# Performance work log

Measured on AMD Instinct MI355X. Metric: run time of the kernel, lower is better.

The kernel has to match this reference:

```python
import jax, jax.numpy as jnp
import numpy as np

RELU_SCALE = 0.25  # const power-of-two activation scale for QuantReLU (uint4)
DN = ('NCHW', 'OIHW', 'NCHW')
BN_EPS = 1e-5


def ste_round(x):
    # straight-through-estimator round (brevitas RoundSte)
    return x + jax.lax.stop_gradient(jnp.round(x) - x)


def fq_signed(x, bits):
    # per-tensor symmetric fixed-point fake quant with power-of-two scale
    # (Int8WeightPerTensorFixedPoint / Int8ActPerTensorFixedPoint at bit_width=bits)
    n = 2.0 ** (bits - 1) - 1.0
    m = jnp.maximum(jnp.max(jnp.abs(x)), 1e-8)
    s = jax.lax.stop_gradient(jnp.exp2(jnp.ceil(jnp.log2(m / n))))
    return jnp.clip(ste_round(x / s), -n - 1.0, n) * s


def quant_relu4(x):
    # QuantReLU: uint4, CONST power-of-two scale
    return jnp.clip(ste_round(x / RELU_SCALE), 0.0, 15.0) * RELU_SCALE


def bn(x, g, b, m, v):
    # inference-form BatchNorm2d (running stats)
    inv = g * jax.lax.rsqrt(v + BN_EPS)
    return x * inv[None, :, None, None] + (b - m * inv)[None, :, None, None]


def qconv(x, w, stride, groups):
    # QuantConv2d: fake-quant input (int4) and weight (int4), then conv
    xq = fq_signed(x, 4)
    wq = fq_signed(w, 4)
    pad = 'VALID' if w.shape[-1] == 1 else ((1, 1), (1, 1))
    return jax.lax.conv_general_dilated(
        xq, wq, (stride, stride), pad,
        dimension_numbers=DN, feature_group_count=groups)


def setup_inputs() -> dict:
    key = jax.random.key(0)
    ks = jax.random.split(key, 24)
    B, Cin, H, W = 32, 64, 56, 56
    expansion, Cout = 6, 96
    P = expansion * Cin  # 384

    def bn_params(i, C):
        g = jax.random.uniform(ks[i], (C,), minval=0.5, maxval=1.5)
        b = jax.random.normal(ks[i + 1], (C,)) * 0.1
        m = jax.random.normal(ks[i + 2], (C,)) * 0.1
        v = jax.random.uniform(ks[i + 3], (C,), minval=0.5, maxval=1.5)
        return g, b, m, v

    x = jax.random.normal(ks[0], (B, Cin, H, W), dtype=jnp.float32)
    w1 = jax.random.normal(ks[1], (P, Cin, 1, 1), dtype=jnp.float32) * 0.1
    w2 = jax.random.normal(ks[2], (P, 1, 3, 3), dtype=jnp.float32) * 0.1
    w3 = jax.random.normal(ks[3], (Cout, P, 1, 1), dtype=jnp.float32) * 0.1
    ws = jax.random.normal(ks[4], (Cout, Cin, 1, 1), dtype=jnp.float32) * 0.1
    g1, b1, m1, v1 = bn_params(5, P)
    g2, b2, m2, v2 = bn_params(9, P)
    g3, b3, m3, v3 = bn_params(13, Cout)
    gs, bs, ms, vs = bn_params(17, Cout)
    return {
        'x': x,
        'w1': w1, 'g1': g1, 'b1': b1, 'm1': m1, 'v1': v1,
        'w2': w2, 'g2': g2, 'b2': b2, 'm2': m2, 'v2': v2,
        'w3': w3, 'g3': g3, 'b3': b3, 'm3': m3, 'v3': v3,
        'ws': ws, 'gs': gs, 'bs': bs, 'ms': ms, 'vs': vs,
    }


def reference(x, w1, g1, b1, m1, v1, w2, g2, b2, m2, v2,
              w3, g3, b3, m3, v3, ws, gs, bs, ms, vs):
    P = w1.shape[0]
    # expand 1x1 -> BN -> QuantReLU
    out = quant_relu4(bn(qconv(x, w1, 1, 1), g1, b1, m1, v1))
    # depthwise 3x3 (stride=1) -> BN -> QuantReLU
    out = quant_relu4(bn(qconv(out, w2, 1, P), g2, b2, m2, v2))
    # project 1x1 with int8 output_quant -> BN
    out = bn(fq_signed(qconv(out, w3, 1, 1), 8), g3, b3, m3, v3)
    # shortcut: 1x1 quant conv (int4 output_quant) -> BN  (stride==1, Cin!=Cout)
    sc = bn(fq_signed(qconv(x, ws, 1, 1), 4), gs, bs, ms, vs)
    return quant_relu4(out + sc)
```

## Files before the change

### kernel.cpp

```cpp
#include <hip/hip_runtime.h>
#include <stdint.h>

#define B_  32
#define CIN 64
#define H_  56
#define W_  56
#define HW_ 3136
#define P_  384
#define CO_ 96

__device__ __forceinline__ float pot_scale(float m, float n) {
    float q = fmaxf(m, 1e-8f) / n;
    int e; float f = frexpf(q, &e);
    return ldexpf(1.0f, (f == 0.5f) ? (e - 1) : e);
}

__device__ __forceinline__ int dot8(int a, int b, int c) {
#if __has_builtin(__builtin_amdgcn_sdot8)
    return __builtin_amdgcn_sdot8(a, b, c, false);
#else
#pragma unroll
    for (int j = 0; j < 8; j++) {
        int av = (a << (28 - 4 * j)) >> 28;
        int bv = (b << (28 - 4 * j)) >> 28;
        c += av * bv;
    }
    return c;
#endif
}

__device__ __forceinline__ int iclamp(int v, int lo, int hi) { return min(max(v, lo), hi); }

__device__ __forceinline__ unsigned build_lut(float r, int lo) {
    unsigned v = 0;
#pragma unroll
    for (int L = 0; L < 8; L++)
        v |= (unsigned)min((int)rintf(__fmul_rn((float)(lo + L), r)), 7) << (4 * L);
    return v;
}
__device__ __forceinline__ int lut1(unsigned lo, unsigned hi, int L) {
    unsigned sel = (L & 8) ? hi : lo;
    return (int)((sel >> ((L & 7) * 4)) & 7u);
}
__device__ __forceinline__ unsigned lutn4(unsigned lo, unsigned hi, unsigned v) {
    return (unsigned)lut1(lo, hi, (int)(v & 0xffu))
         | ((unsigned)lut1(lo, hi, (int)((v >> 8) & 0xffu)) << 4)
         | ((unsigned)lut1(lo, hi, (int)((v >> 16) & 0xffu)) << 8)
         | ((unsigned)lut1(lo, hi, (int)((v >> 24) & 0xffu)) << 12);
}

__device__ __forceinline__ int block_max(int v, int* red) {
    int tid = threadIdx.x;
    red[tid] = v; __syncthreads();
    for (int s = 128; s > 0; s >>= 1) {
        if (tid < s) red[tid] = max(red[tid], red[tid + s]);
        __syncthreads();
    }
    int r = red[0];
    __syncthreads();
    return r;
}


__global__ __launch_bounds__(1024) void k_init_bn(
    float* sf, float* bnb,
    const float* g1, const float* b1, const float* m1, const float* v1,
    const float* g2, const float* b2, const float* m2, const float* v2,
    const float* g3, const float* b3, const float* m3, const float* v3,
    const float* gs, const float* bs, const float* ms, const float* vs)
{
    int t = threadIdx.x;
    if (t < 32) ((int*)sf)[t] = 0;
    if (t < 384) {
        float inv = __fmul_rn(g1[t], __fdiv_rn(1.0f, sqrtf(__fadd_rn(v1[t], 1e-5f))));
        bnb[t] = inv;
        bnb[384 + t] = __fsub_rn(b1[t], __fmul_rn(m1[t], inv));
    } else if (t < 768) {
        int i = t - 384;
        float inv = __fmul_rn(g2[i], __fdiv_rn(1.0f, sqrtf(__fadd_rn(v2[i], 1e-5f))));
        bnb[768 + i] = inv;
        bnb[1152 + i] = __fsub_rn(b2[i], __fmul_rn(m2[i], inv));
    } else if (t < 864) {
        int i = t - 768;
        float inv = __fmul_rn(g3[i], __fdiv_rn(1.0f, sqrtf(__fadd_rn(v3[i], 1e-5f))));
        bnb[1536 + i] = inv;
        bnb[1632 + i] = __fsub_rn(b3[i], __fmul_rn(m3[i], inv));
    } else if (t < 960) {
        int i = t - 864;
        float inv = __fmul_rn(gs[i], __fdiv_rn(1.0f, sqrtf(__fadd_rn(vs[i], 1e-5f))));
        bnb[1728 + i] = inv;
        bnb[1824 + i] = __fsub_rn(bs[i], __fmul_rn(ms[i], inv));
    }
}

__global__ __launch_bounds__(256) void k_maxes(
    const float* __restrict__ x, const float* __restrict__ w1,
    const float* __restrict__ w2, const float* __restrict__ w3,
    const float* __restrict__ wsc, float* sf)
{
    __shared__ int red[256];
    int tid = threadIdx.x;
    float m = 0.f;
    if (blockIdx.x < 512) {
        const float4* x4 = (const float4*)x;
        const int n4 = (B_ * CIN * HW_) / 4;
        for (int i = blockIdx.x * 256 + tid; i < n4; i += 512 * 256) {
            float4 v = x4[i];
            m = fmaxf(m, fmaxf(fmaxf(fabsf(v.x), fabsf(v.y)),
                               fmaxf(fabsf(v.z), fabsf(v.w))));
        }
        int bm = block_max(__float_as_int(m), red);
        if (tid == 0) atomicMax((int*)&sf[0], bm);
    } else {
        int seg = blockIdx.x - 512;
        const float* p = seg == 0 ? w1 : seg == 1 ? w2 : seg == 2 ? w3 : wsc;
        int n = seg == 0 ? P_ * CIN : seg == 1 ? P_ * 9 : seg == 2 ? CO_ * P_ : CO_ * CIN;
        for (int i = tid; i < n; i += 256) m = fmaxf(m, fabsf(p[i]));
        int bm = block_max(__float_as_int(m), red);
        if (tid == 0) atomicMax((int*)&sf[1 + seg], bm);
    }
}

__global__ __launch_bounds__(256) void k_quantx(
    const float* __restrict__ x, const float* __restrict__ sf, int* __restrict__ xq4)
{
    int flat = blockIdx.x * 256 + threadIdx.x;
    float rx = 1.0f / pot_scale(sf[0], 7.0f);
    int hw = flat % HW_;
    int c8 = (flat / HW_) & 7;
    int b  = flat / (8 * HW_);
    const float* xp = x + (size_t)(b * 64 + c8 * 8) * HW_ + hw;
    unsigned pk = 0;
#pragma unroll
    for (int j = 0; j < 8; j++) {
        int q = iclamp((int)rintf(__fmul_rn(xp[(size_t)j * HW_], rx)), -8, 7);
        pk |= (unsigned)(q & 0xF) << (4 * j);
    }
    xq4[flat] = (int)pk;
}

__global__ __launch_bounds__(256) void k_quantw(
    const float* __restrict__ w1, const float* __restrict__ w2,
    const float* __restrict__ w3, const float* __restrict__ wsc,
    const float* __restrict__ sf,
    int* __restrict__ w1n, int8_t* __restrict__ w2q,
    int* __restrict__ w3n, int* __restrict__ wsn)
{
    int flat = blockIdx.x * 256 + threadIdx.x;
    if (flat < 3072) {
        int d = flat, co = d & 3, k8 = (d >> 2) & 7, g = d >> 5;
        float r = 1.0f / pot_scale(sf[1], 7.f);
        const float* src = w1 + (4 * g + co) * 64 + 8 * k8;
        unsigned pk = 0;
#pragma unroll
        for (int j = 0; j < 8; j++) {
            int q = iclamp((int)rintf(__fmul_rn(src[j], r)), -8, 7);
            pk |= (unsigned)(q & 0xF) << (4 * j);
        }
        w1n[d] = (int)pk;
    } else if (flat < 7680) {
        int d = flat - 3072, co = d & 3, k8 = (d >> 2) % 48, coq = d / 192;
        float r = 1.0f / pot_scale(sf[3], 7.f);
        const float* src = w3 + (4 * coq + co) * 384 + 8 * k8;
        unsigned pk = 0;
#pragma unroll
        for (int j = 0; j < 8; j++) {
            int q = iclamp((int)rintf(__fmul_rn(src[j], r)), -8, 7);
            pk |= (unsigned)(q & 0xF) << (4 * j);
        }
        w3n[d] = (int)pk;
    } else if (flat < 8448) {
        int d = flat - 7680, co = d & 3, k8 = (d >> 2) & 7, coq = d >> 5;
        float r = 1.0f / pot_scale(sf[4], 7.f);
        const float* src = wsc + (4 * coq + co) * 64 + 8 * k8;
        unsigned pk = 0;
#pragma unroll
        for (int j = 0; j < 8; j++) {
            int q = iclamp((int)rintf(__fmul_rn(src[j], r)), -8, 7);
            pk |= (unsigned)(q & 0xF) << (4 * j);
        }
        wsn[d] = (int)pk;
    } else if (flat < 11904) {
        int i = flat - 8448;
        float r = 1.0f / pot_scale(sf[2], 7.f);
        w2q[i] = (int8_t)iclamp((int)rintf(__fmul_rn(w2[i], r)), -8, 7);
    }
}

__global__ __launch_bounds__(256) void k_conv1(
    const int* __restrict__ xq4, const int4* __restrict__ w1n,
    const int4* __restrict__ wsn,
    const float* __restrict__ sf, const float* __restrict__ bnb,
    unsigned* __restrict__ out1p, int* si)
{
    __shared__ __align__(16) int xs[8 * W_];
    __shared__ int red[256];
    int tid = threadIdx.x;
    int b = blockIdx.x / H_, h = blockIdx.x % H_;
    for (int i = tid; i < 8 * W_; i += 256)
        xs[i] = xq4[((b * 8 + i / W_) * HW_) + h * W_ + (i % W_)];
    float sprod = __fmul_rn(pot_scale(sf[0], 7.f), pot_scale(sf[1], 7.f));
    __syncthreads();
    int lmax = 0;
    for (int qi = tid; qi < 96 * 14; qi += 256) {
        int g = qi / 14, w4 = (qi % 14) * 4;
        int acc[4][4];
#pragma unroll
        for (int c = 0; c < 4; c++)
#pragma unroll
            for (int w = 0; w < 4; w++) acc[c][w] = 0;
        const int4* wp = w1n + g * 8;
#pragma unroll
        for (int k = 0; k < 8; k++) {
            int4 wv = wp[k];
            int4 xv = *(const int4*)&xs[k * W_ + w4];
            acc[0][0] = dot8(xv.x, wv.x, acc[0][0]); acc[0][1] = dot8(xv.y, wv.x, acc[0][1]);
            acc[0][2] = dot8(xv.z, wv.x, acc[0][2]); acc[0][3] = dot8(xv.w, wv.x, acc[0][3]);
            acc[1][0] = dot8(xv.x, wv.y, acc[1][0]); acc[1][1] = dot8(xv.y, wv.y, acc[1][1]);
            acc[1][2] = dot8(xv.z, wv.y, acc[1][2]); acc[1][3] = dot8(xv.w, wv.y, acc[1][3]);
            acc[2][0] = dot8(xv.x, wv.z, acc[2][0]); acc[2][1] = dot8(xv.y, wv.z, acc[2][1]);
            acc[2][2] = dot8(xv.z, wv.z, acc[2][2]); acc[2][3] = dot8(xv.w, wv.z, acc[2][3]);
            acc[3][0] = dot8(xv.x, wv.w, acc[3][0]); acc[3][1] = dot8(xv.y, wv.w, acc[3][1]);
            acc[3][2] = dot8(xv.z, wv.w, acc[3][2]); acc[3][3] = dot8(xv.w, wv.w, acc[3][3]);
        }
        float4 invv = *(const float4*)&bnb[4 * g];
        float4 betv = *(const float4*)&bnb[384 + 4 * g];
        float inva[4] = {invv.x, invv.y, invv.z, invv.w};
        float beta[4] = {betv.x, betv.y, betv.z, betv.w};
        uint4 ov;
        unsigned* op = (unsigned*)&ov;
#pragma unroll
        for (int w = 0; w < 4; w++) {
            unsigned pkd = 0;
#pragma unroll
            for (int c = 0; c < 4; c++) {
                float y = __fadd_rn(__fmul_rn(__fmul_rn((float)acc[c][w], sprod), inva[c]), beta[c]);
                int L = iclamp((int)rintf(__fmul_rn(y, 4.f)), 0, 15);
                lmax = max(lmax, L);
                pkd |= (unsigned)L << (8 * c);
            }
            op[w] = pkd;
        }
        *(uint4*)(out1p + (size_t)(b * 96 + g) * HW_ + h * W_ + w4) = ov;
    }
    int bm = block_max(lmax, red);
    if (tid == 0) atomicMax(&si[5], bm);
    int amax = 0;
    for (int qi = tid; qi < 24 * 14; qi += 256) {
        int coq = qi / 14, w4 = (qi % 14) * 4;
        int acc[4][4];
#pragma unroll
        for (int c = 0; c < 4; c++)
#pragma unroll
            for (int w = 0; w < 4; w++) acc[c][w] = 0;
        const int4* wp = wsn + coq * 8;
#pragma unroll
        for (int k = 0; k < 8; k++) {
            int4 wv = wp[k];
            int4 xv = *(const int4*)&xs[k * W_ + w4];
            acc[0][0] = dot8(xv.x, wv.x, acc[0][0]); acc[0][1] = dot8(xv.y, wv.x, acc[0][1]);
            acc[0][2] = dot8(xv.z, wv.x, acc[0][2]); acc[0][3] = dot8(xv.w, wv.x, acc[0][3]);
            acc[1][0] = dot8(xv.x, wv.y, acc[1][0]); acc[1][1] = dot8(xv.y, wv.y, acc[1][1]);
            acc[1][2] = dot8(xv.z, wv.y, acc[1][2]); acc[1][3] = dot8(xv.w, wv.y, acc[1][3]);
            acc[2][0] = dot8(xv.x, wv.z, acc[2][0]); acc[2][1] = dot8(xv.y, wv.z, acc[2][1]);
            acc[2][2] = dot8(xv.z, wv.z, acc[2][2]); acc[2][3] = dot8(xv.w, wv.z, acc[2][3]);
            acc[3][0] = dot8(xv.x, wv.w, acc[3][0]); acc[3][1] = dot8(xv.y, wv.w, acc[3][1]);
            acc[3][2] = dot8(xv.z, wv.w, acc[3][2]); acc[3][3] = dot8(xv.w, wv.w, acc[3][3]);
        }
#pragma unroll
        for (int c = 0; c < 4; c++)
            amax = max(amax, max(max(abs(acc[c][0]), abs(acc[c][1])),
                                 max(abs(acc[c][2]), abs(acc[c][3]))));
    }
    bm = block_max(amax, red);
    if (tid == 0) atomicMax(&si[8], bm);
}

__global__ __launch_bounds__(256) void k_conv2(
    const unsigned* __restrict__ out1p, const int8_t* __restrict__ w2q,
    const float* __restrict__ sf, int* si,
    const float* __restrict__ bnb, unsigned* __restrict__ out2p)
{
    __shared__ int plane[58 * 58];
    __shared__ int red[256];
    int tid = threadIdx.x;
    int b = blockIdx.x / 96, g = blockIdx.x % 96;
    float s_a2 = pot_scale(0.25f * (float)si[5], 7.f);
    float r2 = 0.25f / s_a2;
    float sprod = __fmul_rn(s_a2, pot_scale(sf[2], 7.f));
    unsigned lutlo = build_lut(r2, 0), luthi = build_lut(r2, 8);
    const unsigned* src = out1p + (size_t)(b * 96 + g) * HW_;
    for (int i = tid; i < 58 * 58; i += 256) {
        int r = i / 58, c = i % 58;
        int pv = 0;
        if (r >= 1 && r <= 56 && c >= 1 && c <= 56) {
            unsigned v = src[(r - 1) * W_ + (c - 1)];
            pv = lut1(lutlo, luthi, (int)(v & 0xffu))
               | (lut1(lutlo, luthi, (int)((v >> 8) & 0xffu)) << 8)
               | (lut1(lutlo, luthi, (int)((v >> 16) & 0xffu)) << 16)
               | (lut1(lutlo, luthi, (int)((v >> 24) & 0xffu)) << 24);
        }
        plane[i] = pv;
    }
    int wv[4][9];
#pragma unroll
    for (int c = 0; c < 4; c++)
#pragma unroll
        for (int t = 0; t < 9; t++) wv[c][t] = (int)w2q[(4 * g + c) * 9 + t];
    float4 invv = *(const float4*)&bnb[768 + 4 * g];
    float4 betv = *(const float4*)&bnb[1152 + 4 * g];
    float inva[4] = {invv.x, invv.y, invv.z, invv.w};
    float beta[4] = {betv.x, betv.y, betv.z, betv.w};
    __syncthreads();
    int lmax = 0;
    unsigned* dst = out2p + (size_t)(b * 96 + g) * HW_;
    for (int i = tid; i < HW_; i += 256) {
        int oh = i / W_, ow = i % W_;
        int acc[4] = {0, 0, 0, 0};
#pragma unroll
        for (int j = 0; j < 3; j++) {
#pragma unroll
            for (int l = 0; l < 3; l++) {
                int pv = plane[(oh + j) * 58 + ow + l];
                int t = j * 3 + l;
                acc[0] += (pv & 0xff)         * wv[0][t];
                acc[1] += ((pv >> 8) & 0xff)  * wv[1][t];
                acc[2] += ((pv >> 16) & 0xff) * wv[2][t];
                acc[3] += ((pv >> 24) & 0xff) * wv[3][t];
            }
        }
        unsigned pkd = 0;
#pragma unroll
        for (int c = 0; c < 4; c++) {
            float y = __fadd_rn(__fmul_rn(__fmul_rn((float)acc[c], sprod), inva[c]), beta[c]);
            int L = iclamp((int)rintf(__fmul_rn(y, 4.f)), 0, 15);
            lmax = max(lmax, L);
            pkd |= (unsigned)L << (8 * c);
        }
        dst[i] = pkd;
    }
    int bm = block_max(lmax, red);
    if (tid == 0) atomicMax(&si[6], bm);
}

__global__ __launch_bounds__(256) void k_conv3(
    const unsigned* __restrict__ out2p, const int4* __restrict__ w3n,
    const float* __restrict__ sf, int* si,
    int16_t* __restrict__ acc3)
{
    __shared__ __align__(16) int a3s[2 * 48 * W_];
    __shared__ int red[256];
    int tid = threadIdx.x;
    int b = blockIdx.x / 28, h0 = (blockIdx.x % 28) * 2;
    float s_a3 = pot_scale(0.25f * (float)si[6], 7.f);
    float r3 = 0.25f / s_a3;
    unsigned lutlo = build_lut(r3, 0), luthi = build_lut(r3, 8);
    for (int i = tid; i < 2 * 48 * W_; i += 256) {
        int row = i / (48 * W_), rem = i % (48 * W_), c8 = rem / W_, w = rem % W_;
        size_t base = (size_t)(b * 96 + c8 * 2) * HW_ + (h0 + row) * W_ + w;
        unsigned v0 = out2p[base], v1 = out2p[base + HW_];
        a3s[i] = (int)(lutn4(lutlo, luthi, v0) | (lutn4(lutlo, luthi, v1) << 16));
    }
    __syncthreads();
    int amax = 0;
    for (int qi = tid; qi < 672; qi += 256) {
        int row = qi / 336, rem2 = qi % 336, coq = rem2 / 14, w4 = (rem2 % 14) * 4;
        int acc[4][4];
#pragma unroll
        for (int c = 0; c < 4; c++)
#pragma unroll
            for (int w = 0; w < 4; w++) acc[c][w] = 0;
        const int4* wp = w3n + coq * 48;
        const int* ap = a3s + row * 48 * W_ + w4;
#pragma unroll 6
        for (int k = 0; k < 48; k++) {
            int4 wv = wp[k];
            int4 av = *(const int4*)(ap + k * W_);
            acc[0][0] = dot8(av.x, wv.x, acc[0][0]); acc[0][1] = dot8(av.y, wv.x, acc[0][1]);
            acc[0][2] = dot8(av.z, wv.x, acc[0][2]); acc[0][3] = dot8(av.w, wv.x, acc[0][3]);
            acc[1][0] = dot8(av.x, wv.y, acc[1][0]); acc[1][1] = dot8(av.y, wv.y, acc[1][1]);
            acc[1][2] = dot8(av.z, wv.y, acc[1][2]); acc[1][3] = dot8(av.w, wv.y, acc[1][3]);
            acc[2][0] = dot8(av.x, wv.z, acc[2][0]); acc[2][1] = dot8(av.y, wv.z, acc[2][1]);
            acc[2][2] = dot8(av.z, wv.z, acc[2][2]); acc[2][3] = dot8(av.w, wv.z, acc[2][3]);
            acc[3][0] = dot8(av.x, wv.w, acc[3][0]); acc[3][1] = dot8(av.y, wv.w, acc[3][1]);
            acc[3][2] = dot8(av.z, wv.w, acc[3][2]); acc[3][3] = dot8(av.w, wv.w, acc[3][3]);
        }
#pragma unroll
        for (int c = 0; c < 4; c++) {
            int co = coq * 4 + c;
            amax = max(amax, max(max(abs(acc[c][0]), abs(acc[c][1])),
                                 max(abs(acc[c][2]), abs(acc[c][3]))));
            short4 st = make_short4((short)acc[c][0], (short)acc[c][1],
                                    (short)acc[c][2], (short)acc[c][3]);
            *(short4*)(acc3 + (size_t)(b * CO_ + co) * HW_ + (h0 + row) * W_ + w4) = st;
        }
    }
    int bm = block_max(amax, red);
    if (tid == 0) atomicMax(&si[7], bm);
}

__global__ __launch_bounds__(256) void k_final(
    const int* __restrict__ xq4, const int4* __restrict__ wsn,
    const int16_t* __restrict__ acc3, const float* __restrict__ sf,
    const int* __restrict__ si, const float* __restrict__ bnb,
    float* __restrict__ dout)
{
    __shared__ __align__(16) int xs[8 * W_];
    int tid = threadIdx.x;
    int b = blockIdx.x / H_, h = blockIdx.x % H_;
    for (int i = tid; i < 8 * W_; i += 256)
        xs[i] = xq4[((b * 8 + i / W_) * HW_) + h * W_ + (i % W_)];
    float s_a3   = pot_scale(0.25f * (float)si[6], 7.f);
    float sprod3 = __fmul_rn(s_a3, pot_scale(sf[3], 7.f));
    float s_q3   = pot_scale(__fmul_rn(sprod3, (float)si[7]), 127.f);
    float rq3    = sprod3 / s_q3;
    float sprods = __fmul_rn(pot_scale(sf[0], 7.f), pot_scale(sf[4], 7.f));
    float s_qs   = pot_scale(__fmul_rn(sprods, (float)si[8]), 7.f);
    float rqs    = sprods / s_qs;
    __syncthreads();
    for (int qi = tid; qi < 24 * 14; qi += 256) {
        int coq = qi / 14, w4 = (qi % 14) * 4;
        int acc[4][4];
#pragma unroll
        for (int c = 0; c < 4; c++)
#pragma unroll
            for (int w = 0; w < 4; w++) acc[c][w] = 0;
        const int4* wp = wsn + coq * 8;
#pragma unroll
        for (int k = 0; k < 8; k++) {
            int4 wv = wp[k];
            int4 xv = *(const int4*)&xs[k * W_ + w4];
            acc[0][0] = dot8(xv.x, wv.x, acc[0][0]); acc[0][1] = dot8(xv.y, wv.x, acc[0][1]);
            acc[0][2] = dot8(xv.z, wv.x, acc[0][2]); acc[0][3] = dot8(xv.w, wv.x, acc[0][3]);
            acc[1][0] = dot8(xv.x, wv.y, acc[1][0]); acc[1][1] = dot8(xv.y, wv.y, acc[1][1]);
            acc[1][2] = dot8(xv.z, wv.y, acc[1][2]); acc[1][3] = dot8(xv.w, wv.y, acc[1][3]);
            acc[2][0] = dot8(xv.x, wv.z, acc[2][0]); acc[2][1] = dot8(xv.y, wv.z, acc[2][1]);
            acc[2][2] = dot8(xv.z, wv.z, acc[2][2]); acc[2][3] = dot8(xv.w, wv.z, acc[2][3]);
            acc[3][0] = dot8(xv.x, wv.w, acc[3][0]); acc[3][1] = dot8(xv.y, wv.w, acc[3][1]);
            acc[3][2] = dot8(xv.z, wv.w, acc[3][2]); acc[3][3] = dot8(xv.w, wv.w, acc[3][3]);
        }
        float4 inv3v = *(const float4*)&bnb[1536 + 4 * coq];
        float4 bet3v = *(const float4*)&bnb[1632 + 4 * coq];
        float4 invSv = *(const float4*)&bnb[1728 + 4 * coq];
        float4 betSv = *(const float4*)&bnb[1824 + 4 * coq];
        float inv3a[4] = {inv3v.x, inv3v.y, inv3v.z, inv3v.w};
        float bet3a[4] = {bet3v.x, bet3v.y, bet3v.z, bet3v.w};
        float invSa[4] = {invSv.x, invSv.y, invSv.z, invSv.w};
        float betSa[4] = {betSv.x, betSv.y, betSv.z, betSv.w};
#pragma unroll
        for (int c = 0; c < 4; c++) {
            int co = coq * 4 + c;
            size_t idx = (size_t)(b * CO_ + co) * HW_ + h * W_ + w4;
            short4 c3 = *(const short4*)(acc3 + idx);
            int c3a[4] = {c3.x, c3.y, c3.z, c3.w};
            float4 o4;
            float* o = (float*)&o4;
#pragma unroll
            for (int j = 0; j < 4; j++) {
                int q3 = iclamp((int)rintf(__fmul_rn((float)c3a[j], rq3)), -128, 127);
                float y3 = __fadd_rn(__fmul_rn(__fmul_rn((float)q3, s_q3), inv3a[c]), bet3a[c]);
                int qs = iclamp((int)rintf(__fmul_rn((float)acc[c][j], rqs)), -8, 7);
                float ys = __fadd_rn(__fmul_rn(__fmul_rn((float)qs, s_qs), invSa[c]), betSa[c]);
                float oo = __fadd_rn(y3, ys);
                int L = iclamp((int)rintf(__fmul_rn(oo, 4.f)), 0, 15);
                o[j] = (float)L * 0.25f;
            }
            *(float4*)(dout + idx) = o4;
        }
    }
}

extern "C" void kernel_launch(void* const* d_in, const int* in_sizes, int n_in,
                              void* d_out, int out_size, void* d_ws, size_t ws_size,
                              hipStream_t stream)
{
    const float* x   = (const float*)d_in[0];
    const float* w1  = (const float*)d_in[1];
    const float* g1  = (const float*)d_in[2];
    const float* b1  = (const float*)d_in[3];
    const float* m1  = (const float*)d_in[4];
    const float* v1  = (const float*)d_in[5];
    const float* w2  = (const float*)d_in[6];
    const float* g2  = (const float*)d_in[7];
    const float* b2  = (const float*)d_in[8];
    const float* m2  = (const float*)d_in[9];
    const float* v2  = (const float*)d_in[10];
    const float* w3  = (const float*)d_in[11];
    const float* g3  = (const float*)d_in[12];
    const float* b3  = (const float*)d_in[13];
    const float* m3  = (const float*)d_in[14];
    const float* v3  = (const float*)d_in[15];
    const float* wsc = (const float*)d_in[16];
    const float* gs  = (const float*)d_in[17];
    const float* bs  = (const float*)d_in[18];
    const float* ms  = (const float*)d_in[19];
    const float* vs  = (const float*)d_in[20];

    char* ws = (char*)d_ws;
    float*    sf    = (float*)ws;
    int*      si    = (int*)ws;
    float*    bnb   = (float*)(ws + 256);
    int*      w1n   = (int*)(ws + 8192);
    int8_t*   w2q   = (int8_t*)(ws + 32768);
    int*      w3n   = (int*)(ws + 36864);
    int*      wsn   = (int*)(ws + 73728);
    int*      xq4   = (int*)(ws + (1u << 20));
    unsigned* out1p = (unsigned*)(ws + (8u << 20));
    int16_t*  acc3  = (int16_t*)(ws + (8u << 20));
    unsigned* out2p = (unsigned*)(ws + (48u << 20));

    k_init_bn<<<1, 1024, 0, stream>>>(sf, bnb, g1, b1, m1, v1, g2, b2, m2, v2,
                                      g3, b3, m3, v3, gs, bs, ms, vs);
    k_maxes<<<516, 256, 0, stream>>>(x, w1, w2, w3, wsc, sf);
    k_quantx<<<3136, 256, 0, stream>>>(x, sf, xq4);
    k_quantw<<<47, 256, 0, stream>>>(w1, w2, w3, wsc, sf, w1n, w2q, w3n, wsn);
    k_conv1<<<B_ * H_, 256, 0, stream>>>(xq4, (const int4*)w1n, (const int4*)wsn,
                                         sf, bnb, out1p, si);
    k_conv2<<<B_ * 96, 256, 0, stream>>>(out1p, w2q, sf, si, bnb, out2p);
    k_conv3<<<B_ * 28, 256, 0, stream>>>(out2p, (const int4*)w3n, sf, si, acc3);
    k_final<<<B_ * H_, 256, 0, stream>>>(xq4, (const int4*)wsn, acc3, sf, si, bnb,
                                         (float*)d_out);
}
```

Measured before the change: 305.1 us.

## Retile conv1/conv2 work, vectorize x quantization, widen max-reduction grid

Several kernels are reworked at once. k_maxes launches more blocks over x. k_quantx handles four pixels per thread with float4 loads and int4 stores. k_conv1 now runs 192 threads, each keeping its group's weights and BN params in registers across seven pixel quads, with a reduction variant that zero-pads the unused shared slots. k_conv2 gives each thread a column and slides a 3x3 register window down rows to reuse loads, and k_conv3 reorders its work index so neighbouring threads share weights. The aim is fewer redundant global and shared loads, at the cost of idle lanes (ow>=56) and extra register use.

```diff
diff --git a/kernel.cpp b/kernel.cpp
--- a/kernel.cpp
+++ b/kernel.cpp
@@ -52,6 +52,20 @@
 __device__ __forceinline__ int block_max(int v, int* red) {
     int tid = threadIdx.x;
     red[tid] = v; __syncthreads();
+    for (int s = 128; s > 0; s >>= 1) {
+        if (tid < s) red[tid] = max(red[tid], red[tid + s]);
+        __syncthreads();
+    }
+    int r = red[0];
+    __syncthreads();
+    return r;
+}
+
+__device__ __forceinline__ int block_max192(int v, int* red) {
+    int tid = threadIdx.x;
+    red[tid] = v;
+    if (tid < 64) red[192 + tid] = 0;
+    __syncthreads();
     for (int s = 128; s > 0; s >>= 1) {
         if (tid < s) red[tid] = max(red[tid], red[tid + s]);
         __syncthreads();
@@ -93,6 +107,7 @@
     }
 }
 
+#define XBLK 2044
 __global__ __launch_bounds__(256) void k_maxes(
     const float* __restrict__ x, const float* __restrict__ w1,
     const float* __restrict__ w2, const float* __restrict__ w3,
@@ -101,10 +116,10 @@
     __shared__ int red[256];
     int tid = threadIdx.x;
     float m = 0.f;
-    if (blockIdx.x < 512) {
+    if (blockIdx.x < XBLK) {
         const float4* x4 = (const float4*)x;
         const int n4 = (B_ * CIN * HW_) / 4;
-        for (int i = blockIdx.x * 256 + tid; i < n4; i += 512 * 256) {
+        for (int i = blockIdx.x * 256 + tid; i < n4; i += XBLK * 256) {
             float4 v = x4[i];
             m = fmaxf(m, fmaxf(fmaxf(fabsf(v.x), fabsf(v.y)),
                                fmaxf(fabsf(v.z), fabsf(v.w))));
@@ -112,7 +127,7 @@
         int bm = block_max(__float_as_int(m), red);
         if (tid == 0) atomicMax((int*)&sf[0], bm);
     } else {
-        int seg = blockIdx.x - 512;
+        int seg = blockIdx.x - XBLK;
         const float* p = seg == 0 ? w1 : seg == 1 ? w2 : seg == 2 ? w3 : wsc;
         int n = seg == 0 ? P_ * CIN : seg == 1 ? P_ * 9 : seg == 2 ? CO_ * P_ : CO_ * CIN;
         for (int i = tid; i < n; i += 256) m = fmaxf(m, fabsf(p[i]));
@@ -124,19 +139,25 @@
 __global__ __launch_bounds__(256) void k_quantx(
     const float* __restrict__ x, const float* __restrict__ sf, int* __restrict__ xq4)
 {
-    int flat = blockIdx.x * 256 + threadIdx.x;
+    int t = blockIdx.x * 256 + threadIdx.x;
     float rx = 1.0f / pot_scale(sf[0], 7.0f);
-    int hw = flat % HW_;
-    int c8 = (flat / HW_) & 7;
-    int b  = flat / (8 * HW_);
-    const float* xp = x + (size_t)(b * 64 + c8 * 8) * HW_ + hw;
-    unsigned pk = 0;
+    int hw4 = (t % 784) * 4;
+    int c8  = (t / 784) & 7;
+    int b   = t / (784 * 8);
+    const float* xp = x + (size_t)(b * 64 + c8 * 8) * HW_ + hw4;
+    unsigned pk[4] = {0, 0, 0, 0};
 #pragma unroll
     for (int j = 0; j < 8; j++) {
-        int q = iclamp((int)rintf(__fmul_rn(xp[(size_t)j * HW_], rx)), -8, 7);
-        pk |= (unsigned)(q & 0xF) << (4 * j);
-    }
-    xq4[flat] = (int)pk;
+        float4 v = *(const float4*)(xp + (size_t)j * HW_);
+        float va[4] = {v.x, v.y, v.z, v.w};
+#pragma unroll
+        for (int w = 0; w < 4; w++) {
+            int q = iclamp((int)rintf(__fmul_rn(va[w], rx)), -8, 7);
+            pk[w] |= (unsigned)(q & 0xF) << (4 * j);
+        }
+    }
+    int4 st = make_int4((int)pk[0], (int)pk[1], (int)pk[2], (int)pk[3]);
+    *(int4*)(xq4 + (size_t)(b * 8 + c8) * HW_ + hw4) = st;
 }
 
 __global__ __launch_bounds__(256) void k_quantw(
@@ -187,7 +208,7 @@
     }
 }
 
-__global__ __launch_bounds__(256) void k_conv1(
+__global__ __launch_bounds__(192) void k_conv1(
     const int* __restrict__ xq4, const int4* __restrict__ w1n,
     const int4* __restrict__ wsn,
     const float* __restrict__ sf, const float* __restrict__ bnb,
@@ -197,19 +218,71 @@
     __shared__ int red[256];
     int tid = threadIdx.x;
     int b = blockIdx.x / H_, h = blockIdx.x % H_;
-    for (int i = tid; i < 8 * W_; i += 256)
+    for (int i = tid; i < 8 * W_; i += 192)
         xs[i] = xq4[((b * 8 + i / W_) * HW_) + h * W_ + (i % W_)];
     float sprod = __fmul_rn(pot_scale(sf[0], 7.f), pot_scale(sf[1], 7.f));
     __syncthreads();
+    int g = tid % 96, half = tid / 96;
+    int4 wreg[8];
+    {
+        const int4* wp = w1n + g * 8;
+#pragma unroll
+        for (int k = 0; k < 8; k++) wreg[k] = wp[k];
+    }
+    float4 invv = *(const float4*)&bnb[4 * g];
+    float4 betv = *(const float4*)&bnb[384 + 4 * g];
+    float inva[4] = {invv.x, invv.y, invv.z, invv.w};
+    float beta[4] = {betv.x, betv.y, betv.z, betv.w};
     int lmax = 0;
-    for (int qi = tid; qi < 96 * 14; qi += 256) {
-        int g = qi / 14, w4 = (qi % 14) * 4;
+    unsigned* dst = out1p + (size_t)(b * 96 + g) * HW_ + h * W_;
+#pragma unroll
+    for (int q = 0; q < 7; q++) {
+        int w4 = half * 28 + q * 4;
         int acc[4][4];
 #pragma unroll
         for (int c = 0; c < 4; c++)
 #pragma unroll
             for (int w = 0; w < 4; w++) acc[c][w] = 0;
-        const int4* wp = w1n + g * 8;
+#pragma unroll
+        for (int k = 0; k < 8; k++) {
+            int4 wv = wreg[k];
+            int4 xv = *(const int4*)&xs[k * W_ + w4];
+            acc[0][0] = dot8(xv.x, wv.x, acc[0][0]); acc[0][1] = dot8(xv.y, wv.x, acc[0][1]);
+            acc[0][2] = dot8(xv.z, wv.x, acc[0][2]); acc[0][3] = dot8(xv.w, wv.x, acc[0][3]);
+            acc[1][0] = dot8(xv.x, wv.y, acc[1][0]); acc[1][1] = dot8(xv.y, wv.y, acc[1][1]);
+            acc[1][2] = dot8(xv.z, wv.y, acc[1][2]); acc[1][3] = dot8(xv.w, wv.y, acc[1][3]);
+            acc[2][0] = dot8(xv.x, wv.z, acc[2][0]); acc[2][1] = dot8(xv.y, wv.z, acc[2][1]);
+            acc[2][2] = dot8(xv.z, wv.z, acc[2][2]); acc[2][3] = dot8(xv.w, wv.z, acc[2][3]);
+            acc[3][0] = dot8(xv.x, wv.w, acc[3][0]); acc[3][1] = dot8(xv.y, wv.w, acc[3][1]);
+            acc[3][2] = dot8(xv.z, wv.w, acc[3][2]); acc[3][3] = dot8(xv.w, wv.w, acc[3][3]);
+        }
+        uint4 ov;
+        unsigned* op = (unsigned*)&ov;
+#pragma unroll
+        for (int w = 0; w < 4; w++) {
+            unsigned pkd = 0;
+#pragma unroll
+            for (int c = 0; c < 4; c++) {
+                float y = __fadd_rn(__fmul_rn(__fmul_rn((float)acc[c][w], sprod), inva[c]), beta[c]);
+                int L = iclamp((int)rintf(__fmul_rn(y, 4.f)), 0, 15);
+                lmax = max(lmax, L);
+                pkd |= (unsigned)L << (8 * c);
+            }
+            op[w] = pkd;
+        }
+        *(uint4*)(dst + w4) = ov;
+    }
+    int bm = block_max192(lmax, red);
+    if (tid == 0) atomicMax(&si[5], bm);
+    int amax = 0;
+    for (int qi = tid; qi < 336; qi += 192) {
+        int coq = qi / 14, w4 = (qi % 14) * 4;
+        int acc[4][4];
+#pragma unroll
+        for (int c = 0; c < 4; c++)
+#pragma unroll
+            for (int w = 0; w < 4; w++) acc[c][w] = 0;
+        const int4* wp = wsn + coq * 8;
 #pragma unroll
         for (int k = 0; k < 8; k++) {
             int4 wv = wp[k];
@@ -223,56 +296,12 @@
             acc[3][0] = dot8(xv.x, wv.w, acc[3][0]); acc[3][1] = dot8(xv.y, wv.w, acc[3][1]);
             acc[3][2] = dot8(xv.z, wv.w, acc[3][2]); acc[3][3] = dot8(xv.w, wv.w, acc[3][3]);
         }
-        float4 invv = *(const float4*)&bnb[4 * g];
-        float4 betv = *(const float4*)&bnb[384 + 4 * g];
-        float inva[4] = {invv.x, invv.y, invv.z, invv.w};
-        float beta[4] = {betv.x, betv.y, betv.z, betv.w};
-        uint4 ov;
-        unsigned* op = (unsigned*)&ov;
-#pragma unroll
-        for (int w = 0; w < 4; w++) {
-            unsigned pkd = 0;
-#pragma unroll
-            for (int c = 0; c < 4; c++) {
-                float y = __fadd_rn(__fmul_rn(__fmul_rn((float)acc[c][w], sprod), inva[c]), beta[c]);
-                int L = iclamp((int)rintf(__fmul_rn(y, 4.f)), 0, 15);
-                lmax = max(lmax, L);
-                pkd |= (unsigned)L << (8 * c);
-            }
-            op[w] = pkd;
-        }
-        *(uint4*)(out1p + (size_t)(b * 96 + g) * HW_ + h * W_ + w4) = ov;
-    }
-    int bm = block_max(lmax, red);
-    if (tid == 0) atomicMax(&si[5], bm);
-    int amax = 0;
-    for (int qi = tid; qi < 24 * 14; qi += 256) {
-        int coq = qi / 14, w4 = (qi % 14) * 4;
-        int acc[4][4];
-#pragma unroll
-        for (int c = 0; c < 4; c++)
-#pragma unroll
-            for (int w = 0; w < 4; w++) acc[c][w] = 0;
-        const int4* wp = wsn + coq * 8;
-#pragma unroll
-        for (int k = 0; k < 8; k++) {
-            int4 wv = wp[k];
-            int4 xv = *(const int4*)&xs[k * W_ + w4];
-            acc[0][0] = dot8(xv.x, wv.x, acc[0][0]); acc[0][1] = dot8(xv.y, wv.x, acc[0][1]);
-            acc[0][2] = dot8(xv.z, wv.x, acc[0][2]); acc[0][3] = dot8(xv.w, wv.x, acc[0][3]);
-            acc[1][0] = dot8(xv.x, wv.y, acc[1][0]); acc[1][1] = dot8(xv.y, wv.y, acc[1][1]);
-            acc[1][2] = dot8(xv.z, wv.y, acc[1][2]); acc[1][3] = dot8(xv.w, wv.y, acc[1][3]);
-            acc[2][0] = dot8(xv.x, wv.z, acc[2][0]); acc[2][1] = dot8(xv.y, wv.z, acc[2][1]);
-            acc[2][2] = dot8(xv.z, wv.z, acc[2][2]); acc[2][3] = dot8(xv.w, wv.z, acc[2][3]);
-            acc[3][0] = dot8(xv.x, wv.w, acc[3][0]); acc[3][1] = dot8(xv.y, wv.w, acc[3][1]);
-            acc[3][2] = dot8(xv.z, wv.w, acc[3][2]); acc[3][3] = dot8(xv.w, wv.w, acc[3][3]);
-        }
 #pragma unroll
         for (int c = 0; c < 4; c++)
             amax = max(amax, max(max(abs(acc[c][0]), abs(acc[c][1])),
                                  max(abs(acc[c][2]), abs(acc[c][3]))));
     }
-    bm = block_max(amax, red);
+    bm = block_max192(amax, red);
     if (tid == 0) atomicMax(&si[8], bm);
 }
 
@@ -313,31 +342,34 @@
     float beta[4] = {betv.x, betv.y, betv.z, betv.w};
     __syncthreads();
     int lmax = 0;
-    unsigned* dst = out2p + (size_t)(b * 96 + g) * HW_;
-    for (int i = tid; i < HW_; i += 256) {
-        int oh = i / W_, ow = i % W_;
-        int acc[4] = {0, 0, 0, 0};
-#pragma unroll
-        for (int j = 0; j < 3; j++) {
-#pragma unroll
-            for (int l = 0; l < 3; l++) {
-                int pv = plane[(oh + j) * 58 + ow + l];
-                int t = j * 3 + l;
-                acc[0] += (pv & 0xff)         * wv[0][t];
-                acc[1] += ((pv >> 8) & 0xff)  * wv[1][t];
-                acc[2] += ((pv >> 16) & 0xff) * wv[2][t];
-                acc[3] += ((pv >> 24) & 0xff) * wv[3][t];
+    int ow = tid & 63, seg = tid >> 6;
+    if (ow < 56) {
+        int oh0 = seg * 14;
+        const int* pr = plane + ow;
+        unsigned* dst = out2p + (size_t)(b * 96 + g) * HW_ + ow;
+        int p00 = pr[oh0 * 58],       p01 = pr[oh0 * 58 + 1],       p02 = pr[oh0 * 58 + 2];
+        int p10 = pr[(oh0 + 1) * 58], p11 = pr[(oh0 + 1) * 58 + 1], p12 = pr[(oh0 + 1) * 58 + 2];
+#pragma unroll 2
+        for (int oh = oh0; oh < oh0 + 14; oh++) {
+            int p20 = pr[(oh + 2) * 58], p21 = pr[(oh + 2) * 58 + 1], p22 = pr[(oh + 2) * 58 + 2];
+            unsigned pkd = 0;
+#pragma unroll
+            for (int c = 0; c < 4; c++) {
+                int sh = 8 * c;
+                int acc = ((p00 >> sh) & 0xff) * wv[c][0] + ((p01 >> sh) & 0xff) * wv[c][1]
+                        + ((p02 >> sh) & 0xff) * wv[c][2] + ((p10 >> sh) & 0xff) * wv[c][3]
+                        + ((p11 >> sh) & 0xff) * wv[c][4] + ((p12 >> sh) & 0xff) * wv[c][5]
+                        + ((p20 >> sh) & 0xff) * wv[c][6] + ((p21 >> sh) & 0xff) * wv[c][7]
+                        + ((p22 >> sh) & 0xff) * wv[c][8];
+                float y = __fadd_rn(__fmul_rn(__fmul_rn((float)acc, sprod), inva[c]), beta[c]);
+                int L = iclamp((int)rintf(__fmul_rn(y, 4.f)), 0, 15);
+                lmax = max(lmax, L);
+                pkd |= (unsigned)L << sh;
             }
-        }
-        unsigned pkd = 0;
-#pragma unroll
-        for (int c = 0; c < 4; c++) {
-            float y = __fadd_rn(__fmul_rn(__fmul_rn((float)acc[c], sprod), inva[c]), beta[c]);
-            int L = iclamp((int)rintf(__fmul_rn(y, 4.f)), 0, 15);
-            lmax = max(lmax, L);
-            pkd |= (unsigned)L << (8 * c);
-        }
-        dst[i] = pkd;
+            dst[oh * W_] = pkd;
+            p00 = p10; p01 = p11; p02 = p12;
+            p10 = p20; p11 = p21; p12 = p22;
+        }
     }
     int bm = block_max(lmax, red);
     if (tid == 0) atomicMax(&si[6], bm);
@@ -364,7 +396,7 @@
     __syncthreads();
     int amax = 0;
     for (int qi = tid; qi < 672; qi += 256) {
-        int row = qi / 336, rem2 = qi % 336, coq = rem2 / 14, w4 = (rem2 % 14) * 4;
+        int coq = qi / 28, rem2 = qi % 28, row = rem2 / 14, w4 = (rem2 % 14) * 4;
         int acc[4][4];
 #pragma unroll
         for (int c = 0; c < 4; c++)
@@ -511,10 +543,10 @@
 
     k_init_bn<<<1, 1024, 0, stream>>>(sf, bnb, g1, b1, m1, v1, g2, b2, m2, v2,
                                       g3, b3, m3, v3, gs, bs, ms, vs);
-    k_maxes<<<516, 256, 0, stream>>>(x, w1, w2, w3, wsc, sf);
-    k_quantx<<<3136, 256, 0, stream>>>(x, sf, xq4);
+    k_maxes<<<XBLK + 4, 256, 0, stream>>>(x, w1, w2, w3, wsc, sf);
+    k_quantx<<<784, 256, 0, stream>>>(x, sf, xq4);
     k_quantw<<<47, 256, 0, stream>>>(w1, w2, w3, wsc, sf, w1n, w2q, w3n, wsn);
-    k_conv1<<<B_ * H_, 256, 0, stream>>>(xq4, (const int4*)w1n, (const int4*)wsn,
+    k_conv1<<<B_ * H_, 192, 0, stream>>>(xq4, (const int4*)w1n, (const int4*)wsn,
                                          sf, bnb, out1p, si);
     k_conv2<<<B_ * 96, 256, 0, stream>>>(out1p, w2q, sf, si, bnb, out2p);
     k_conv3<<<B_ * 28, 256, 0, stream>>>(out2p, (const int4*)w3n, sf, si, acc3);
```

Result: slower. 313.9 us (+2.9%).
